# Kernel optimization log

Measured on AMD Instinct MI355X. Metric: run time of the kernel, lower is better.

## Reference

```python
import jax, jax.numpy as jnp
import numpy as np

N = 100000  # nodes
E = 1600000  # edges (avg degree 16)
F = 128  # input feature dim
D = 64   # output dim
BN_EPS = 1e-3  # keras BatchNormalization default epsilon


def setup_inputs() -> dict:
    key = jax.random.key(0)
    k1, k2, k3, k4, k5 = jax.random.split(key, 5)
    x = jax.random.normal(k1, (N, F), dtype=jnp.float32)
    kernel = jax.random.normal(k2, (F, D), dtype=jnp.float32) * (1.0 / np.sqrt(F))
    edge_vals = jax.random.uniform(k3, (E,), dtype=jnp.float32)
    rows = jax.random.randint(k4, (E,), 0, N, dtype=jnp.int32)
    cols = jax.random.randint(k5, (E,), 0, N, dtype=jnp.int32)
    return {"x": x, "kernel": kernel, "edge_vals": edge_vals,
            "rows": rows, "cols": cols, "nodes_num": N}


def reference(x, kernel, edge_vals, rows, cols, nodes_num):
    # BatchNormalization (fresh layer -> gamma=1, beta=0, batch statistics over axis 0)
    mean = jnp.mean(x, axis=0)
    var = jnp.var(x, axis=0)
    xn = (x - mean) * jax.lax.rsqrt(var + BN_EPS)
    # dense projection: [N, F] @ [F, D] -> [N, D]
    h = xn @ kernel
    # tf.sparse.softmax == per-row softmax over the nonzero adjacency values
    row_max = jax.ops.segment_max(edge_vals, rows, num_segments=nodes_num)
    e = jnp.exp(edge_vals - row_max[rows])
    row_sum = jax.ops.segment_sum(e, rows, num_segments=nodes_num)
    attn = e / row_sum[rows]  # [E]
    # sparse-dense matmul: out[i] = sum_j attn_ij * h[j]
    msgs = attn[:, None] * h[cols]  # [E, D] gather
    out = jax.ops.segment_sum(msgs, rows, num_segments=nodes_num)  # scatter-add
    return jnp.tanh(out)
```

## Files before the change

### kernel.cpp

```cpp
#include <hip/hip_runtime.h>
#include <math.h>

#define F 128
#define D 64
#define BSHIFT 9
#define CHUNK 4096
#define BCAP 16384

__global__ __launch_bounds__(256) void k_stats(const float* __restrict__ x,
                                               float* __restrict__ stats, int N) {
    int tid = threadIdx.x;
    int f = tid & 127;
    int rowOff = tid >> 7;
    float s = 0.f, sq = 0.f;
    for (int r = blockIdx.x * 2 + rowOff; r < N; r += gridDim.x * 2) {
        float v = x[(size_t)r * F + f];
        s += v; sq += v * v;
    }
    __shared__ float ls[256], lq[256];
    ls[tid] = s; lq[tid] = sq;
    __syncthreads();
    if (tid < 128) {
        atomicAdd(&stats[f],       ls[tid] + ls[tid + 128]);
        atomicAdd(&stats[128 + f], lq[tid] + lq[tid + 128]);
    }
}

__global__ __launch_bounds__(128) void k_prep(const float* __restrict__ stats,
                                              const float* __restrict__ W,
                                              float* __restrict__ Kp,
                                              float* __restrict__ bias, int N) {
    __shared__ float mean_s[F], rs_s[F];
    int t = threadIdx.x;
    float invN = 1.0f / (float)N;
    float m   = stats[t] * invN;
    float var = stats[128 + t] * invN - m * m;
    float rs  = rsqrtf(var + 1e-3f);
    mean_s[t] = m; rs_s[t] = rs;
    __syncthreads();
    for (int i = 0; i < 64; ++i) {
        int idx = t + 128 * i;
        int f = idx >> 6;
        Kp[idx] = rs_s[f] * W[idx];
    }
    if (t < D) {
        float b = 0.f;
        for (int f = 0; f < F; ++f) b -= mean_s[f] * rs_s[f] * W[f * D + t];
        bias[t] = b;
    }
}

__global__ __launch_bounds__(256) void k_gemm(const float* __restrict__ x,
                                              const float* __restrict__ Kp,
                                              const float* __restrict__ bias,
                                              float* __restrict__ h, int N) {
    __shared__ float Ks[F * D];
    __shared__ float4 xs4[4][256];
    __shared__ float bs[D];
    int tid = threadIdx.x;
    for (int i = tid; i < F * D / 4; i += 256)
        ((float4*)Ks)[i] = ((const float4*)Kp)[i];
    if (tid < D) bs[tid] = bias[tid];

    int wave = tid >> 6, lane = tid & 63;
    int base = blockIdx.x * 32 + wave * 8;
    const float4* xsrc = (const float4*)(x + (size_t)base * F);
    xs4[wave][lane]       = xsrc[lane];
    xs4[wave][lane + 64]  = xsrc[lane + 64];
    xs4[wave][lane + 128] = xsrc[lane + 128];
    xs4[wave][lane + 192] = xsrc[lane + 192];
    __syncthreads();

    float acc[8];
    #pragma unroll
    for (int r = 0; r < 8; ++r) acc[r] = bs[lane];

    const float4* xrow = xs4[wave];
    #pragma unroll 4
    for (int f4 = 0; f4 < 32; ++f4) {
        float k0 = Ks[(4 * f4 + 0) * D + lane];
        float k1 = Ks[(4 * f4 + 1) * D + lane];
        float k2 = Ks[(4 * f4 + 2) * D + lane];
        float k3 = Ks[(4 * f4 + 3) * D + lane];
        #pragma unroll
        for (int r = 0; r < 8; ++r) {
            float4 a = xrow[r * 32 + f4];
            acc[r] += a.x * k0 + a.y * k1 + a.z * k2 + a.w * k3;
        }
    }
    #pragma unroll
    for (int r = 0; r < 8; ++r)
        h[(size_t)(base + r) * D + lane] = acc[r];
}

__global__ __launch_bounds__(256) void k_count(const int* __restrict__ rows,
                                               int* __restrict__ cnt, int E) {
    int e = blockIdx.x * 256 + threadIdx.x;
    if (e < E) atomicAdd(&cnt[rows[e]], 1);
}

__global__ __launch_bounds__(1024) void k_scan1(const int* __restrict__ cnt,
                                                int* __restrict__ startm,
                                                int* __restrict__ partials, int N) {
    __shared__ int s0[1024], s1[1024];
    int t = threadIdx.x, i = blockIdx.x * 1024 + t;
    int v = (i < N) ? cnt[i] : 0;
    s0[t] = v;
    __syncthreads();
    int* a = s0; int* b = s1;
    for (int off = 1; off < 1024; off <<= 1) {
        int val = a[t] + ((t >= off) ? a[t - off] : 0);
        b[t] = val;
        __syncthreads();
        int* tmp = a; a = b; b = tmp;
    }
    if (i < N) startm[i] = a[t] - v;
    if (t == 1023) partials[blockIdx.x] = a[1023];
}

__global__ __launch_bounds__(128) void k_scan2(int* __restrict__ partials, int NB) {
    __shared__ int s0[128], s1[128];
    int t = threadIdx.x;
    int v = (t < NB) ? partials[t] : 0;
    s0[t] = v;
    __syncthreads();
    int* a = s0; int* b = s1;
    for (int off = 1; off < 128; off <<= 1) {
        int val = a[t] + ((t >= off) ? a[t - off] : 0);
        b[t] = val;
        __syncthreads();
        int* tmp = a; a = b; b = tmp;
    }
    if (t < NB) partials[t] = a[t] - v;
}

__global__ __launch_bounds__(1024) void k_scan3(int* __restrict__ startm,
                                                const int* __restrict__ partials, int N) {
    int i = blockIdx.x * 1024 + threadIdx.x;
    if (i < N) startm[i] += partials[blockIdx.x];
}

__global__ __launch_bounds__(256) void k_binprep(const int* __restrict__ startm,
                                                 int* __restrict__ bincur,
                                                 int nbins, int N) {
    int b = threadIdx.x;
    if (b < nbins) bincur[b] = startm[b << BSHIFT];
}

__global__ __launch_bounds__(256) void k_blocksortA(const int* __restrict__ rows,
                                                    const int* __restrict__ cols,
                                                    const float* __restrict__ ev,
                                                    int* __restrict__ bincur,
                                                    float4* __restrict__ ce_tmp, int E) {
    __shared__ int lcnt[256], lofs[256], gbase[256];
    __shared__ int sA[256], sB[256];
    __shared__ unsigned short binof[CHUNK];
    __shared__ float4 buf[CHUNK];
    int tid = threadIdx.x;
    int e0 = blockIdx.x * CHUNK, e1 = min(E, e0 + CHUNK);

    lcnt[tid] = 0;
    __syncthreads();
    for (int e = e0 + tid; e < e1; e += 256)
        atomicAdd(&lcnt[rows[e] >> BSHIFT], 1);
    __syncthreads();
    sA[tid] = lcnt[tid];
    __syncthreads();
    int* a = sA; int* b = sB;
    for (int off = 1; off < 256; off <<= 1) {
        int val = a[tid] + ((tid >= off) ? a[tid - off] : 0);
        b[tid] = val;
        __syncthreads();
        int* tmp = a; a = b; b = tmp;
    }
    lofs[tid] = a[tid] - lcnt[tid];
    __syncthreads();
    lcnt[tid] = lofs[tid];
    __syncthreads();
    for (int e = e0 + tid; e < e1; e += 256) {
        int r = rows[e];
        int bin = r >> BSHIFT;
        int slot = atomicAdd(&lcnt[bin], 1);
        buf[slot] = make_float4(__int_as_float(r), __int_as_float(cols[e]), ev[e], 0.f);
        binof[slot] = (unsigned short)bin;
    }
    __syncthreads();
    {
        int c = lcnt[tid] - lofs[tid];
        if (c > 0) gbase[tid] = atomicAdd(&bincur[tid], c);
    }
    __syncthreads();
    int n = e1 - e0;
    for (int s = tid; s < n; s += 256) {
        int bin = binof[s];
        ce_tmp[gbase[bin] + (s - lofs[bin])] = buf[s];
    }
}

__global__ __launch_bounds__(256) void k_binsortB(const float4* __restrict__ ce_tmp,
                                                  const int* __restrict__ startm,
                                                  float2* __restrict__ ce, int N, int E) {
    __shared__ float2 lbuf[BCAP];
    __shared__ int cur[1 << BSHIFT];
    int tid = threadIdx.x;
    int r0 = blockIdx.x << BSHIFT;
    int r1 = min(N, r0 + (1 << BSHIFT));
    int gbeg = startm[r0];
    int gend = (r1 < N) ? startm[r1] : E;
    int count = gend - gbeg;
    for (int i = tid; i < (1 << BSHIFT); i += 256) {
        int r = r0 + i;
        cur[i] = (r < r1) ? (startm[r] - gbeg) : count;
    }
    __syncthreads();
    if (count <= BCAP) {
        for (int k = tid; k < count; k += 256) {
            float4 t = ce_tmp[gbeg + k];
            int row = __float_as_int(t.x);
            int slot = atomicAdd(&cur[row - r0], 1);
            lbuf[slot] = make_float2(t.y, t.z);
        }
        __syncthreads();
        for (int k = tid; k < count; k += 256)
            ce[gbeg + k] = lbuf[k];
    } else {
        for (int k = tid; k < count; k += 256) {
            float4 t = ce_tmp[gbeg + k];
            int row = __float_as_int(t.x);
            int slot = atomicAdd(&cur[row - r0], 1);
            ce[gbeg + slot] = make_float2(t.y, t.z);
        }
    }
}

__global__ __launch_bounds__(256) void k_agg(const int* __restrict__ startm,
                                             const int* __restrict__ cnt,
                                             const float2* __restrict__ ce,
                                             const float* __restrict__ h,
                                             float* __restrict__ out, int N) {
    int wid = threadIdx.x >> 6, lane = threadIdx.x & 63;
    int r = blockIdx.x * 4 + wid;
    if (r >= N) return;
    int base = startm[r];
    int nd   = cnt[r];
    int end  = base + nd;

    if (nd <= 64) {
        float2 e = make_float2(0.f, -INFINITY);
        if (lane < nd) e = ce[base + lane];
        float m = e.y;
        #pragma unroll
        for (int off = 32; off; off >>= 1) m = fmaxf(m, __shfl_xor(m, off));
        float w = (lane < nd) ? __expf(e.y - m) : 0.f;
        float s = w;
        #pragma unroll
        for (int off = 32; off; off >>= 1) s += __shfl_xor(s, off);
        w *= (nd > 0) ? (1.f / s) : 0.f;
        int c = __float_as_int(e.x) * D;

        float acc = 0.f;
        for (int j = 0; j < nd; j += 8) {
            int   c0 = __shfl(c, j + 0), c1 = __shfl(c, j + 1);
            int   c2 = __shfl(c, j + 2), c3 = __shfl(c, j + 3);
            int   c4 = __shfl(c, j + 4), c5 = __shfl(c, j + 5);
            int   c6 = __shfl(c, j + 6), c7 = __shfl(c, j + 7);
            float w0 = __shfl(w, j + 0), w1 = __shfl(w, j + 1);
            float w2 = __shfl(w, j + 2), w3 = __shfl(w, j + 3);
            float w4 = __shfl(w, j + 4), w5 = __shfl(w, j + 5);
            float w6 = __shfl(w, j + 6), w7 = __shfl(w, j + 7);
            acc += w0 * h[c0 + lane] + w1 * h[c1 + lane]
                 + w2 * h[c2 + lane] + w3 * h[c3 + lane];
            acc += w4 * h[c4 + lane] + w5 * h[c5 + lane]
                 + w6 * h[c6 + lane] + w7 * h[c7 + lane];
        }
        out[(size_t)r * D + lane] = tanhf(acc);
    } else {
        float m = -INFINITY;
        for (int i = base + lane; i < end; i += 64) m = fmaxf(m, ce[i].y);
        #pragma unroll
        for (int off = 32; off; off >>= 1) m = fmaxf(m, __shfl_xor(m, off));
        float s = 0.f;
        for (int i = base + lane; i < end; i += 64) s += __expf(ce[i].y - m);
        #pragma unroll
        for (int off = 32; off; off >>= 1) s += __shfl_xor(s, off);
        float inv = 1.f / s;
        float acc = 0.f;
        for (int i = base; i < end; ++i) {
            float2 t = ce[i];
            acc += __expf(t.y - m) * inv * h[(size_t)__float_as_int(t.x) * D + lane];
        }
        out[(size_t)r * D + lane] = tanhf(acc);
    }
}

__global__ __launch_bounds__(256) void k_rowmax(const float* __restrict__ ev,
                                                const int* __restrict__ rows,
                                                float* __restrict__ rmax, int E) {
    int i = blockIdx.x * 256 + threadIdx.x;
    if (i < E)
        atomicMax((unsigned int*)&rmax[rows[i]], __float_as_uint(ev[i]));
}

__global__ __launch_bounds__(256) void k_rowsum(const float* __restrict__ ev,
                                                const int* __restrict__ rows,
                                                const float* __restrict__ rmax,
                                                float* __restrict__ rsum, int E) {
    int i = blockIdx.x * 256 + threadIdx.x;
    if (i < E) {
        int r = rows[i];
        atomicAdd(&rsum[r], __expf(ev[i] - rmax[r]));
    }
}

__global__ __launch_bounds__(256) void k_scatter(const float* __restrict__ ev,
                                                 const int* __restrict__ rows,
                                                 const int* __restrict__ cols,
                                                 const float* __restrict__ rmax,
                                                 const float* __restrict__ rsum,
                                                 const float* __restrict__ h,
                                                 float* __restrict__ out, int E) {
    int lane = threadIdx.x & 63;
    int e = blockIdx.x * 4 + (threadIdx.x >> 6);
    if (e < E) {
        int r = rows[e], c = cols[e];
        float w = __expf(ev[e] - rmax[r]) / rsum[r];
        atomicAdd(&out[(size_t)r * D + lane], w * h[(size_t)c * D + lane]);
    }
}

__global__ __launch_bounds__(256) void k_tanh(float* __restrict__ out, int n4) {
    for (int i = blockIdx.x * 256 + threadIdx.x; i < n4; i += gridDim.x * 256) {
        float4 v = ((float4*)out)[i];
        v.x = tanhf(v.x); v.y = tanhf(v.y);
        v.z = tanhf(v.z); v.w = tanhf(v.w);
        ((float4*)out)[i] = v;
    }
}

extern "C" void kernel_launch(void* const* d_in, const int* in_sizes, int n_in,
                              void* d_out, int out_size, void* d_ws, size_t ws_size,
                              hipStream_t stream) {
    const float* x    = (const float*)d_in[0];
    const float* W    = (const float*)d_in[1];
    const float* ev   = (const float*)d_in[2];
    const int*   rows = (const int*)d_in[3];
    const int*   cols = (const int*)d_in[4];
    int N = in_sizes[0] / F;
    int E = in_sizes[2];
    float* out = (float*)d_out;
    float* ws  = (float*)d_ws;

    size_t off = 0;
    float* stats = ws + off; off += 256;
    float* Kp    = ws + off; off += F * D;
    float* bias  = ws + off; off += 64;
    off = (off + 255) & ~(size_t)255;

    int nbins = (N + (1 << BSHIFT) - 1) >> BSHIFT;
    int*   cnt      = (int*)(ws + off);   off += N;
    int*   startm   = (int*)(ws + off);   off += N;
    int*   partials = (int*)(ws + off);   off += 128;
    int*   bincur   = (int*)(ws + off);   off += 256;
    off = (off + 255) & ~(size_t)255;
    float2* ce      = (float2*)(ws + off); off += (size_t)2 * E;
    size_t hfloats  = ((size_t)N * D > (size_t)4 * E) ? (size_t)N * D : (size_t)4 * E;
    float* h        = ws + off;            off += hfloats;
    float4* ce_tmp  = (float4*)h;
    size_t need_csr = off * sizeof(float);

    hipMemsetAsync(stats, 0, 256 * sizeof(float), stream);
    k_stats<<<512, 256, 0, stream>>>(x, stats, N);
    k_prep <<<1, 128, 0, stream>>>(stats, W, Kp, bias, N);

    if (need_csr <= ws_size && nbins <= 256) {
        hipMemsetAsync(cnt, 0, (size_t)N * sizeof(int), stream);
        k_count<<<(E + 255) / 256, 256, 0, stream>>>(rows, cnt, E);
        int NB = (N + 1023) / 1024;
        k_scan1<<<NB, 1024, 0, stream>>>(cnt, startm, partials, N);
        k_scan2<<<1, 128, 0, stream>>>(partials, NB);
        k_scan3<<<NB, 1024, 0, stream>>>(startm, partials, N);
        k_binprep<<<1, 256, 0, stream>>>(startm, bincur, nbins, N);
        k_blocksortA<<<(E + CHUNK - 1) / CHUNK, 256, 0, stream>>>(rows, cols, ev, bincur, ce_tmp, E);
        k_binsortB<<<nbins, 256, 0, stream>>>(ce_tmp, startm, ce, N, E);
        k_gemm<<<N / 32, 256, 0, stream>>>(x, Kp, bias, h, N);
        k_agg <<<(N + 3) / 4, 256, 0, stream>>>(startm, cnt, ce, h, out, N);
    } else {
        size_t o2 = (256 + F * D + 64 + 255) & ~(size_t)255;
        float* rmax = ws + o2;  o2 += N;
        float* rsum = ws + o2;  o2 += N;
        float* h2   = ws + o2;  o2 += (size_t)N * D;
        hipMemsetAsync(rmax, 0, (size_t)2 * N * sizeof(float), stream);
        hipMemsetAsync(out, 0, (size_t)out_size * sizeof(float), stream);
        k_gemm  <<<N / 32, 256, 0, stream>>>(x, Kp, bias, h2, N);
        k_rowmax<<<(E + 255) / 256, 256, 0, stream>>>(ev, rows, rmax, E);
        k_rowsum<<<(E + 255) / 256, 256, 0, stream>>>(ev, rows, rmax, rsum, E);
        k_scatter<<<(E + 3) / 4, 256, 0, stream>>>(ev, rows, cols, rmax, rsum, h2, out, E);
        k_tanh  <<<2048, 256, 0, stream>>>(out, (N * D) / 4);
    }
}
```

Measured before the change: 384.5 us.

## Replace per-row count and global scan with bin histogram and in-bin row offsets

Drops the per-row atomic count over all edges, the three-stage global prefix scan over N rows and the bin-prep kernel. In their place, a shared-memory bin histogram and a single 256-entry bin scan feed the block sort. Each bin block in k_binsortB now builds its own per-row histogram and scan, then writes startm and cnt. This cuts global atomics, launches and memset traffic, at the cost of an extra pass over ce_tmp inside each bin block.

```diff
diff --git a/kernel.cpp b/kernel.cpp
--- a/kernel.cpp
+++ b/kernel.cpp
@@ -5,6 +5,7 @@
 #define D 64
 #define BSHIFT 9
 #define CHUNK 4096
+#define HCHUNK 8192
 #define BCAP 16384
 
 __global__ __launch_bounds__(256) void k_stats(const float* __restrict__ x,
@@ -93,58 +94,39 @@
         h[(size_t)(base + r) * D + lane] = acc[r];
 }
 
-__global__ __launch_bounds__(256) void k_count(const int* __restrict__ rows,
-                                               int* __restrict__ cnt, int E) {
-    int e = blockIdx.x * 256 + threadIdx.x;
-    if (e < E) atomicAdd(&cnt[rows[e]], 1);
-}
-
-__global__ __launch_bounds__(1024) void k_scan1(const int* __restrict__ cnt,
-                                                int* __restrict__ startm,
-                                                int* __restrict__ partials, int N) {
-    __shared__ int s0[1024], s1[1024];
-    int t = threadIdx.x, i = blockIdx.x * 1024 + t;
-    int v = (i < N) ? cnt[i] : 0;
+__global__ __launch_bounds__(256) void k_binhist(const int* __restrict__ rows,
+                                                 int* __restrict__ bincnt, int E) {
+    __shared__ int lh[256];
+    int tid = threadIdx.x;
+    lh[tid] = 0;
+    __syncthreads();
+    int e0 = blockIdx.x * HCHUNK, e1 = min(E, e0 + HCHUNK);
+    for (int e = e0 + tid; e < e1; e += 256)
+        atomicAdd(&lh[rows[e] >> BSHIFT], 1);
+    __syncthreads();
+    int c = lh[tid];
+    if (c > 0) atomicAdd(&bincnt[tid], c);
+}
+
+__global__ __launch_bounds__(256) void k_binscan(const int* __restrict__ bincnt,
+                                                 int* __restrict__ binstart,
+                                                 int* __restrict__ bincur, int E) {
+    __shared__ int s0[256], s1[256];
+    int t = threadIdx.x;
+    int v = bincnt[t];
     s0[t] = v;
     __syncthreads();
     int* a = s0; int* b = s1;
-    for (int off = 1; off < 1024; off <<= 1) {
+    for (int off = 1; off < 256; off <<= 1) {
         int val = a[t] + ((t >= off) ? a[t - off] : 0);
         b[t] = val;
         __syncthreads();
         int* tmp = a; a = b; b = tmp;
     }
-    if (i < N) startm[i] = a[t] - v;
-    if (t == 1023) partials[blockIdx.x] = a[1023];
-}
-
-__global__ __launch_bounds__(128) void k_scan2(int* __restrict__ partials, int NB) {
-    __shared__ int s0[128], s1[128];
-    int t = threadIdx.x;
-    int v = (t < NB) ? partials[t] : 0;
-    s0[t] = v;
-    __syncthreads();
-    int* a = s0; int* b = s1;
-    for (int off = 1; off < 128; off <<= 1) {
-        int val = a[t] + ((t >= off) ? a[t - off] : 0);
-        b[t] = val;
-        __syncthreads();
-        int* tmp = a; a = b; b = tmp;
-    }
-    if (t < NB) partials[t] = a[t] - v;
-}
-
-__global__ __launch_bounds__(1024) void k_scan3(int* __restrict__ startm,
-                                                const int* __restrict__ partials, int N) {
-    int i = blockIdx.x * 1024 + threadIdx.x;
-    if (i < N) startm[i] += partials[blockIdx.x];
-}
-
-__global__ __launch_bounds__(256) void k_binprep(const int* __restrict__ startm,
-                                                 int* __restrict__ bincur,
-                                                 int nbins, int N) {
-    int b = threadIdx.x;
-    if (b < nbins) bincur[b] = startm[b << BSHIFT];
+    int excl = a[t] - v;
+    binstart[t] = excl;
+    bincur[t]   = excl;
+    if (t == 255) binstart[256] = E;
 }
 
 __global__ __launch_bounds__(256) void k_blocksortA(const int* __restrict__ rows,
@@ -198,37 +180,59 @@
 }
 
 __global__ __launch_bounds__(256) void k_binsortB(const float4* __restrict__ ce_tmp,
-                                                  const int* __restrict__ startm,
+                                                  const int* __restrict__ binstart,
+                                                  int* __restrict__ startm,
+                                                  int* __restrict__ cnt,
                                                   float2* __restrict__ ce, int N, int E) {
     __shared__ float2 lbuf[BCAP];
-    __shared__ int cur[1 << BSHIFT];
+    __shared__ int hist[512], ofs[512], ps[256], ps2[256];
     int tid = threadIdx.x;
     int r0 = blockIdx.x << BSHIFT;
-    int r1 = min(N, r0 + (1 << BSHIFT));
-    int gbeg = startm[r0];
-    int gend = (r1 < N) ? startm[r1] : E;
+    int gbeg = binstart[blockIdx.x];
+    int gend = binstart[blockIdx.x + 1];
     int count = gend - gbeg;
-    for (int i = tid; i < (1 << BSHIFT); i += 256) {
+
+    hist[tid] = 0; hist[tid + 256] = 0;
+    __syncthreads();
+    for (int k = tid; k < count; k += 256)
+        atomicAdd(&hist[__float_as_int(ce_tmp[gbeg + k].x) - r0], 1);
+    __syncthreads();
+    int h0 = hist[2 * tid], h1 = hist[2 * tid + 1];
+    ps[tid] = h0 + h1;
+    __syncthreads();
+    int* a = ps; int* b = ps2;
+    for (int off = 1; off < 256; off <<= 1) {
+        int val = a[tid] + ((tid >= off) ? a[tid - off] : 0);
+        b[tid] = val;
+        __syncthreads();
+        int* tmp = a; a = b; b = tmp;
+    }
+    int pexcl = a[tid] - (h0 + h1);
+    ofs[2 * tid]     = pexcl;
+    ofs[2 * tid + 1] = pexcl + h0;
+    __syncthreads();
+    for (int i = tid; i < 512; i += 256) {
         int r = r0 + i;
-        cur[i] = (r < r1) ? (startm[r] - gbeg) : count;
-    }
+        if (r < N) { startm[r] = gbeg + ofs[i]; cnt[r] = hist[i]; }
+    }
+    __syncthreads();
+    hist[2 * tid]     = ofs[2 * tid];
+    hist[2 * tid + 1] = ofs[2 * tid + 1];
     __syncthreads();
     if (count <= BCAP) {
         for (int k = tid; k < count; k += 256) {
-            float4 t = ce_tmp[gbeg + k];
-            int row = __float_as_int(t.x);
-            int slot = atomicAdd(&cur[row - r0], 1);
-            lbuf[slot] = make_float2(t.y, t.z);
+            float4 t4 = ce_tmp[gbeg + k];
+            int slot = atomicAdd(&hist[__float_as_int(t4.x) - r0], 1);
+            lbuf[slot] = make_float2(t4.y, t4.z);
         }
         __syncthreads();
         for (int k = tid; k < count; k += 256)
             ce[gbeg + k] = lbuf[k];
     } else {
         for (int k = tid; k < count; k += 256) {
-            float4 t = ce_tmp[gbeg + k];
-            int row = __float_as_int(t.x);
-            int slot = atomicAdd(&cur[row - r0], 1);
-            ce[gbeg + slot] = make_float2(t.y, t.z);
+            float4 t4 = ce_tmp[gbeg + k];
+            int slot = atomicAdd(&hist[__float_as_int(t4.x) - r0], 1);
+            ce[gbeg + slot] = make_float2(t4.y, t4.z);
         }
     }
 }
@@ -357,10 +361,12 @@
     off = (off + 255) & ~(size_t)255;
 
     int nbins = (N + (1 << BSHIFT) - 1) >> BSHIFT;
+    int*   bincnt   = (int*)(ws + off);   off += 256;
+    int*   binstart = (int*)(ws + off);   off += 257;
+    int*   bincur   = (int*)(ws + off);   off += 256;
+    off = (off + 255) & ~(size_t)255;
+    int*   startm   = (int*)(ws + off);   off += N;
     int*   cnt      = (int*)(ws + off);   off += N;
-    int*   startm   = (int*)(ws + off);   off += N;
-    int*   partials = (int*)(ws + off);   off += 128;
-    int*   bincur   = (int*)(ws + off);   off += 256;
     off = (off + 255) & ~(size_t)255;
     float2* ce      = (float2*)(ws + off); off += (size_t)2 * E;
     size_t hfloats  = ((size_t)N * D > (size_t)4 * E) ? (size_t)N * D : (size_t)4 * E;
@@ -373,15 +379,11 @@
     k_prep <<<1, 128, 0, stream>>>(stats, W, Kp, bias, N);
 
     if (need_csr <= ws_size && nbins <= 256) {
-        hipMemsetAsync(cnt, 0, (size_t)N * sizeof(int), stream);
-        k_count<<<(E + 255) / 256, 256, 0, stream>>>(rows, cnt, E);
-        int NB = (N + 1023) / 1024;
-        k_scan1<<<NB, 1024, 0, stream>>>(cnt, startm, partials, N);
-        k_scan2<<<1, 128, 0, stream>>>(partials, NB);
-        k_scan3<<<NB, 1024, 0, stream>>>(startm, partials, N);
-        k_binprep<<<1, 256, 0, stream>>>(startm, bincur, nbins, N);
+        hipMemsetAsync(bincnt, 0, 256 * sizeof(int), stream);
+        k_binhist<<<(E + HCHUNK - 1) / HCHUNK, 256, 0, stream>>>(rows, bincnt, E);
+        k_binscan<<<1, 256, 0, stream>>>(bincnt, binstart, bincur, E);
         k_blocksortA<<<(E + CHUNK - 1) / CHUNK, 256, 0, stream>>>(rows, cols, ev, bincur, ce_tmp, E);
-        k_binsortB<<<nbins, 256, 0, stream>>>(ce_tmp, startm, ce, N, E);
+        k_binsortB<<<nbins, 256, 0, stream>>>(ce_tmp, binstart, startm, cnt, ce, N, E);
         k_gemm<<<N / 32, 256, 0, stream>>>(x, Kp, bias, h, N);
         k_agg <<<(N + 3) / 4, 256, 0, stream>>>(startm, cnt, ce, h, out, N);
     } else {
```

After: 338.8 us. -11.9%, faster.
